# Performance work log

Measured on AMD Instinct MI355X. Metric: run time of the kernel, lower is better.

## Reference

```python
import jax, jax.numpy as jnp
import numpy as np
from jax import lax

N_NODES = 100000
N_EDGES = 600000  # even: edges stored as consecutive reverse pairs
NODE_F = 64
EDGE_F = 16
EDGE_H = 128
NODE_H = 128
NUM_STEPS = 6


def setup_inputs() -> dict:
    key = jax.random.key(0)
    ks = jax.random.split(key, 16)
    # paired reverse edges: edge 2k is (src,dst), edge 2k+1 is (dst,src)
    src = jax.random.randint(ks[0], (N_EDGES // 2,), 0, N_NODES, dtype=jnp.int32)
    dst = jax.random.randint(ks[1], (N_EDGES // 2,), 0, N_NODES, dtype=jnp.int32)
    from_nodes = jnp.stack([src, dst], axis=1).reshape(-1)
    to_nodes = jnp.stack([dst, src], axis=1).reshape(-1)
    edges = jnp.stack([from_nodes, to_nodes], axis=0)
    return {
        "node_features": jax.random.normal(ks[2], (N_NODES, NODE_F), jnp.float32),
        "edge_features": jax.random.normal(ks[3], (N_EDGES, EDGE_F), jnp.float32),
        "edge_hiddens": jnp.zeros((N_EDGES, EDGE_H), jnp.float32),
        "edges": edges,
        "W1_w": jax.random.normal(ks[4], (NODE_F, EDGE_H), jnp.float32) / np.sqrt(NODE_F),
        "W1_b": jnp.zeros((EDGE_H,), jnp.float32),
        "W2_w": jax.random.normal(ks[5], (EDGE_F, EDGE_H), jnp.float32) / np.sqrt(EDGE_F),
        "W2_b": jnp.zeros((EDGE_H,), jnp.float32),
        "W3_w": jax.random.normal(ks[6], (EDGE_H, EDGE_H), jnp.float32) / np.sqrt(EDGE_H),
        "W3_b": jnp.zeros((EDGE_H,), jnp.float32),
        "U1_w": jax.random.normal(ks[7], (NODE_F, NODE_H), jnp.float32) / np.sqrt(NODE_F),
        "U1_b": jnp.zeros((NODE_H,), jnp.float32),
        "U2_w": jax.random.normal(ks[8], (EDGE_H, NODE_H), jnp.float32) / np.sqrt(EDGE_H),
        "U2_b": jnp.zeros((NODE_H,), jnp.float32),
    }


def reference(node_features, edge_features, edge_hiddens, edges,
              W1_w, W1_b, W2_w, W2_b, W3_w, W3_b, U1_w, U1_b, U2_w, U2_b):
    from_nodes = edges[0]
    to_nodes = edges[1]
    n_edges = edges.shape[1]
    # backlink of edge i is its reverse pair: even i -> i+1, odd i -> i-1
    idx = jnp.arange(n_edges)
    backlink = idx + ((idx + 1) % 2) * 2 - 1

    # loop-invariant terms
    W1_x_u = (node_features @ W1_w + W1_b)[from_nodes]     # [E, EH]
    W2_x_uv = edge_features @ W2_w + W2_b                  # [E, EH]

    def step(h, _):
        # sum edge hiddens by source node, gather back per-edge, drop backlink
        s = jax.ops.segment_sum(h, from_nodes, num_segments=N_NODES)  # [N, EH]
        wu = s[from_nodes] - h[backlink]                               # [E, EH]
        h_new = jax.nn.relu(W1_x_u + W2_x_uv + (wu @ W3_w + W3_b))
        return h_new, None

    edge_h, _ = lax.scan(step, edge_hiddens, None, length=NUM_STEPS)

    U1_x_u = node_features @ U1_w + U1_b                   # [N, NH]
    U2_vu = edge_h @ U2_w + U2_b                           # [E, NH]
    agg = jax.ops.segment_sum(U2_vu, to_nodes, num_segments=N_NODES)
    node_hiddens = jax.nn.relu(U1_x_u + agg)               # [N, NH]
    return node_hiddens
```

## Files before the change

kernel.cpp:

```cpp
#include <hip/hip_runtime.h>
#include <hip/hip_bf16.h>

#define N_NODES 100000
#define N_EDGES 600000
#define SCAN_BLOCKS ((N_NODES + 255) / 256)

typedef __bf16 bf16;
typedef __bf16 bf16x2 __attribute__((ext_vector_type(2)));
typedef __bf16 bf16x4 __attribute__((ext_vector_type(4)));
typedef __bf16 bf16x8 __attribute__((ext_vector_type(8)));
typedef float f32x4 __attribute__((ext_vector_type(4)));

__global__ void deg_hist(const int* __restrict__ from, int* __restrict__ deg, int E) {
    int e = blockIdx.x * blockDim.x + threadIdx.x;
    if (e < E) atomicAdd(&deg[from[e]], 1);
}

__global__ __launch_bounds__(256) void block_sums(
    const int* __restrict__ deg, int* __restrict__ bsum)
{
    __shared__ int s[256];
    int i = blockIdx.x * 256 + threadIdx.x;
    s[threadIdx.x] = (i < N_NODES) ? deg[i] : 0;
    __syncthreads();
    for (int st = 128; st > 0; st >>= 1) {
        if (threadIdx.x < st) s[threadIdx.x] += s[threadIdx.x + st];
        __syncthreads();
    }
    if (threadIdx.x == 0) bsum[blockIdx.x] = s[0];
}

__global__ __launch_bounds__(256) void scan_partials(
    const int* __restrict__ bsum, int* __restrict__ bpref, int* __restrict__ off)
{
    __shared__ int s[SCAN_BLOCKS];
    for (int i = threadIdx.x; i < SCAN_BLOCKS; i += 256) s[i] = bsum[i];
    __syncthreads();
    if (threadIdx.x == 0) {
        int run = 0;
        for (int i = 0; i < SCAN_BLOCKS; i++) { int t = s[i]; s[i] = run; run += t; }
        off[N_NODES] = run;
    }
    __syncthreads();
    for (int i = threadIdx.x; i < SCAN_BLOCKS; i += 256) bpref[i] = s[i];
}

__global__ __launch_bounds__(256) void block_scan(
    const int* __restrict__ deg, const int* __restrict__ bpref,
    int* __restrict__ off, int* __restrict__ cursor)
{
    __shared__ int s[256];
    int i = blockIdx.x * 256 + threadIdx.x;
    int v = (i < N_NODES) ? deg[i] : 0;
    s[threadIdx.x] = v;
    __syncthreads();
    for (int st = 1; st < 256; st <<= 1) {
        int x = (threadIdx.x >= st) ? s[threadIdx.x - st] : 0;
        __syncthreads();
        s[threadIdx.x] += x;
        __syncthreads();
    }
    if (i < N_NODES) {
        int o = bpref[blockIdx.x] + s[threadIdx.x] - v;
        off[i] = o;
        cursor[i] = o;
    }
}

__global__ void scatter_csr(const int* __restrict__ from, int* __restrict__ cursor,
                            int* __restrict__ se, int E) {
    int e = blockIdx.x * blockDim.x + threadIdx.x;
    if (e < E) {
        int p = atomicAdd(&cursor[from[e]], 1);
        se[p] = e;
    }
}

__global__ __launch_bounds__(256) void node_gemm(
    const float* __restrict__ A, const float* __restrict__ B,
    const float* __restrict__ bias, float* __restrict__ C, int M)
{
    __shared__ float As[16][65];
    __shared__ float Bs[16][128];
    int row0 = blockIdx.x * 64;
    int tid = threadIdx.x;
    int tx = tid & 15, ty = tid >> 4;
    float acc[4][8];
    #pragma unroll
    for (int i = 0; i < 4; i++)
        #pragma unroll
        for (int j = 0; j < 8; j++) acc[i][j] = 0.f;

    for (int kk = 0; kk < 64; kk += 16) {
        int m  = tid >> 2;
        int k4 = (tid & 3) * 4;
        float4 v = make_float4(0.f, 0.f, 0.f, 0.f);
        if (row0 + m < M)
            v = *(const float4*)(A + (size_t)(row0 + m) * 64 + kk + k4);
        As[k4 + 0][m] = v.x; As[k4 + 1][m] = v.y;
        As[k4 + 2][m] = v.z; As[k4 + 3][m] = v.w;
        #pragma unroll
        for (int t = 0; t < 2; t++) {
            int id = tid + t * 256;
            int k = id >> 5, n4 = (id & 31) * 4;
            *(float4*)(&Bs[k][n4]) = *(const float4*)(B + (size_t)(kk + k) * 128 + n4);
        }
        __syncthreads();
        #pragma unroll
        for (int k = 0; k < 16; k++) {
            float a[4], b[8];
            #pragma unroll
            for (int i = 0; i < 4; i++) a[i] = As[k][ty * 4 + i];
            #pragma unroll
            for (int j = 0; j < 8; j++) b[j] = Bs[k][tx + j * 16];
            #pragma unroll
            for (int i = 0; i < 4; i++)
                #pragma unroll
                for (int j = 0; j < 8; j++) acc[i][j] += a[i] * b[j];
        }
        __syncthreads();
    }
    #pragma unroll
    for (int i = 0; i < 4; i++) {
        int r = row0 + ty * 4 + i;
        if (r < M) {
            #pragma unroll
            for (int j = 0; j < 8; j++) {
                int c = tx + j * 16;
                C[(size_t)r * 128 + c] = acc[i][j] + bias[c];
            }
        }
    }
}

__global__ __launch_bounds__(256) void base_v2(
    const float* __restrict__ nodeW1, const int* __restrict__ from,
    const float* __restrict__ ef, const float* __restrict__ W2,
    const float* __restrict__ W2b, const float* __restrict__ W3b,
    bf16* __restrict__ baseB)
{
    int tid = threadIdx.x;
    int c0 = (tid & 31) * 4;
    int sub = tid >> 5;
    float4 w[16];
    #pragma unroll
    for (int k = 0; k < 16; k++) w[k] = *(const float4*)(W2 + k * 128 + c0);
    float4 bias;
    {
        float4 a = *(const float4*)(W2b + c0);
        float4 b = *(const float4*)(W3b + c0);
        bias = make_float4(a.x + b.x, a.y + b.y, a.z + b.z, a.w + b.w);
    }
    #pragma unroll 1
    for (int it = 0; it < 64; ++it) {
        int e = blockIdx.x * 512 + it * 8 + sub;
        if (e >= N_EDGES) break;
        const float* efr = ef + (size_t)e * 16;
        float4 nv = *(const float4*)(nodeW1 + (size_t)from[e] * 128 + c0);
        float4 acc = make_float4(bias.x + nv.x, bias.y + nv.y,
                                 bias.z + nv.z, bias.w + nv.w);
        #pragma unroll
        for (int k = 0; k < 16; k++) {
            float s = efr[k];
            acc.x += s * w[k].x; acc.y += s * w[k].y;
            acc.z += s * w[k].z; acc.w += s * w[k].w;
        }
        bf16x4 o;
        o[0] = (bf16)acc.x; o[1] = (bf16)acc.y; o[2] = (bf16)acc.z; o[3] = (bf16)acc.w;
        *(bf16x4*)(baseB + (size_t)e * 128 + c0) = o;
    }
}

__global__ __launch_bounds__(256) void prep_weights(
    const float* __restrict__ W3, const float* __restrict__ U2,
    bf16* __restrict__ W3T, bf16* __restrict__ U2T)
{
    int i = blockIdx.x * 256 + threadIdx.x;
    if (i < 128 * 128) {
        int k = i >> 7, n = i & 127;
        W3T[n * 128 + k] = (bf16)W3[k * 128 + n];
        U2T[n * 128 + k] = (bf16)U2[k * 128 + n];
    }
}

__global__ __launch_bounds__(256) void edge_mfma(
    const bf16* __restrict__ baseB, const bf16* __restrict__ gbuf,
    const bf16* __restrict__ Sprev, const int* __restrict__ from,
    const bf16* __restrict__ BT, bf16* __restrict__ gout, int fused)
{
    __shared__ bf16 As[64][136];
    __shared__ bf16 Bs[128][136];
    int row0 = blockIdx.x * 64;
    int tid = threadIdx.x;

    #pragma unroll
    for (int t = 0; t < 8; t++) {
        int cid = tid + t * 256;
        int brow = cid >> 4, bcol = (cid & 15) * 8;
        *(bf16x8*)&Bs[brow][bcol] = *(const bf16x8*)(BT + (size_t)brow * 128 + bcol);
    }

    int r  = tid >> 2;
    int e  = row0 + r;
    int c0 = (tid & 3) * 32;
    if (!fused) {
        #pragma unroll
        for (int cc = 0; cc < 32; cc += 8) {
            int c = c0 + cc;
            bf16x8 bb = *(const bf16x8*)(baseB + (size_t)e * 128 + c);
            bf16x8 o;
            #pragma unroll
            for (int j = 0; j < 8; j++) o[j] = (bf16)fmaxf((float)bb[j], 0.f);
            *(bf16x8*)&As[r][c] = o;
        }
    } else {
        int fe = from[e];
        const bf16* sr = Sprev + (size_t)fe * 128;
        const bf16* gr = gbuf + (size_t)(e ^ 1) * 128;
        #pragma unroll
        for (int cc = 0; cc < 32; cc += 8) {
            int c = c0 + cc;
            bf16x8 bb = *(const bf16x8*)(baseB + (size_t)e * 128 + c);
            bf16x8 gg = *(const bf16x8*)(gr + c);
            bf16x8 ss = *(const bf16x8*)(sr + c);
            bf16x8 o;
            #pragma unroll
            for (int j = 0; j < 8; j++) {
                float v = (float)bb[j] + (float)ss[j] - (float)gg[j];
                o[j] = (bf16)fmaxf(v, 0.f);
            }
            *(bf16x8*)&As[r][c] = o;
        }
    }
    __syncthreads();

    int wave = tid >> 6, lane = tid & 63;
    int quad = lane >> 4, mr = lane & 15;
    int m0 = wave * 16;
    f32x4 acc[8];
    #pragma unroll
    for (int n = 0; n < 8; n++) acc[n] = (f32x4){0.f, 0.f, 0.f, 0.f};
    #pragma unroll
    for (int kt = 0; kt < 4; kt++) {
        bf16x8 a = *(const bf16x8*)&As[m0 + mr][kt * 32 + quad * 8];
        #pragma unroll
        for (int n = 0; n < 8; n++) {
            bf16x8 b = *(const bf16x8*)&Bs[n * 16 + mr][kt * 32 + quad * 8];
            acc[n] = __builtin_amdgcn_mfma_f32_16x16x32_bf16(a, b, acc[n], 0, 0, 0);
        }
    }

    #pragma unroll
    for (int n = 0; n < 8; n++) {
        int col = n * 16 + mr;
        #pragma unroll
        for (int reg = 0; reg < 4; reg++) {
            int rr = row0 + m0 + quad * 4 + reg;
            gout[(size_t)rr * 128 + col] = (bf16)acc[n][reg];
        }
    }
}

template<int FINAL>
__global__ __launch_bounds__(256) void segsum(
    const bf16* __restrict__ g, const int* __restrict__ off,
    const int* __restrict__ se, bf16* __restrict__ Sout, float* __restrict__ aggout)
{
    int n = blockIdx.x * 4 + (threadIdx.x >> 6);
    if (n >= N_NODES) return;
    int lane = threadIdx.x & 63;
    int o0 = off[n], o1 = off[n + 1];
    float a0 = 0.f, a1 = 0.f;
    for (int i = o0; i < o1; ++i) {
        int e = se[i] ^ FINAL;
        bf16x2 v = *(const bf16x2*)(g + (size_t)e * 128 + lane * 2);
        a0 += (float)v[0];
        a1 += (float)v[1];
    }
    if (FINAL) {
        *(float2*)(aggout + (size_t)n * 128 + lane * 2) = make_float2(a0, a1);
    } else {
        bf16x2 o; o[0] = (bf16)a0; o[1] = (bf16)a1;
        *(bf16x2*)(Sout + (size_t)n * 128 + lane * 2) = o;
    }
}

__global__ __launch_bounds__(256) void final_out(
    const float* __restrict__ U1x, const float* __restrict__ agg,
    const int* __restrict__ deg, const float* __restrict__ U2b,
    float* __restrict__ out)
{
    int gid = blockIdx.x * 256 + threadIdx.x;
    int n  = gid >> 5;
    if (n >= N_NODES) return;
    int c4 = gid & 31;
    float d = (float)deg[n];
    float4 a  = *(const float4*)(U1x + (size_t)n * 128 + c4 * 4);
    float4 ag = *(const float4*)(agg + (size_t)n * 128 + c4 * 4);
    float4 ub = *(const float4*)(U2b + c4 * 4);
    float4 r;
    r.x = fmaxf(a.x + ag.x + d * ub.x, 0.f);
    r.y = fmaxf(a.y + ag.y + d * ub.y, 0.f);
    r.z = fmaxf(a.z + ag.z + d * ub.z, 0.f);
    r.w = fmaxf(a.w + ag.w + d * ub.w, 0.f);
    *(float4*)(out + (size_t)n * 128 + c4 * 4) = r;
}

extern "C" void kernel_launch(void* const* d_in, const int* in_sizes, int n_in,
                              void* d_out, int out_size, void* d_ws, size_t ws_size,
                              hipStream_t stream) {
    const float* nf  = (const float*)d_in[0];
    const float* ef  = (const float*)d_in[1];
    const int* edges = (const int*)d_in[3];
    const int* from  = edges;
    const float* W1w = (const float*)d_in[4];
    const float* W1b = (const float*)d_in[5];
    const float* W2w = (const float*)d_in[6];
    const float* W2b = (const float*)d_in[7];
    const float* W3w = (const float*)d_in[8];
    const float* W3b = (const float*)d_in[9];
    const float* U1w = (const float*)d_in[10];
    const float* U1b = (const float*)d_in[11];
    const float* U2w = (const float*)d_in[12];
    const float* U2b = (const float*)d_in[13];
    float* out = (float*)d_out;

    const size_t NODE_MAT = (size_t)N_NODES * 128;
    const size_t EDGE_MAT = (size_t)N_EDGES * 128;
    char* w = (char*)d_ws;
    float* nodeW1 = (float*)w; w += NODE_MAT * 4;
    float* agg    = (float*)w; w += NODE_MAT * 4;
    bf16*  S      = (bf16*)w;  w += NODE_MAT * 2;
    bf16*  baseB  = (bf16*)w;  w += EDGE_MAT * 2;
    bf16*  gbuf   = (bf16*)w;  w += EDGE_MAT * 2;
    bf16*  W3T    = (bf16*)w;  w += 128 * 128 * 2;
    bf16*  U2T    = (bf16*)w;  w += 128 * 128 * 2;
    int*   deg    = (int*)w;   w += (size_t)N_NODES * 4;
    int*   off    = (int*)w;   w += (size_t)(N_NODES + 1) * 4;
    int*   cursor = (int*)w;   w += (size_t)N_NODES * 4;
    int*   bsum   = (int*)w;   w += (size_t)SCAN_BLOCKS * 4;
    int*   bpref  = (int*)w;   w += (size_t)SCAN_BLOCKS * 4;
    int*   se     = (int*)w;   w += (size_t)N_EDGES * 4;

    hipMemsetAsync(deg, 0, (size_t)N_NODES * 4, stream);
    deg_hist<<<(N_EDGES + 255) / 256, 256, 0, stream>>>(from, deg, N_EDGES);
    block_sums<<<SCAN_BLOCKS, 256, 0, stream>>>(deg, bsum);
    scan_partials<<<1, 256, 0, stream>>>(bsum, bpref, off);
    block_scan<<<SCAN_BLOCKS, 256, 0, stream>>>(deg, bpref, off, cursor);
    scatter_csr<<<(N_EDGES + 255) / 256, 256, 0, stream>>>(from, cursor, se, N_EDGES);

    prep_weights<<<(128 * 128 + 255) / 256, 256, 0, stream>>>(W3w, U2w, W3T, U2T);
    node_gemm<<<(N_NODES + 63) / 64, 256, 0, stream>>>(nf, W1w, W1b, nodeW1, N_NODES);
    base_v2<<<(N_EDGES + 511) / 512, 256, 0, stream>>>(nodeW1, from, ef, W2w, W2b, W3b, baseB);

    edge_mfma<<<N_EDGES / 64, 256, 0, stream>>>(baseB, gbuf, S, from, W3T, gbuf, 0);
    segsum<0><<<(N_NODES + 3) / 4, 256, 0, stream>>>(gbuf, off, se, S, agg);
    for (int it = 1; it < 5; ++it) {
        edge_mfma<<<N_EDGES / 64, 256, 0, stream>>>(baseB, gbuf, S, from, W3T, gbuf, 1);
        segsum<0><<<(N_NODES + 3) / 4, 256, 0, stream>>>(gbuf, off, se, S, agg);
    }
    edge_mfma<<<N_EDGES / 64, 256, 0, stream>>>(baseB, gbuf, S, from, U2T, gbuf, 1);
    segsum<1><<<(N_NODES + 3) / 4, 256, 0, stream>>>(gbuf, off, se, S, agg);

    node_gemm<<<(N_NODES + 63) / 64, 256, 0, stream>>>(nf, U1w, U1b, nodeW1, N_NODES);
    final_out<<<(N_NODES * 32 + 255) / 256, 256, 0, stream>>>(nodeW1, agg, deg, U2b, out);
}
```

Before: 1.777 ms.

## Permute edges into CSR order so segment sums stream contiguous rows

Edges are reordered by source node via a rank map, so base terms and per-step hidden buffers live in CSR-sorted order. The per-step segment sum then reads contiguous rows instead of gathering through the edge list. The reverse-edge read becomes an indexed gather through a precomputed backlink map. Hidden buffers are double-buffered, which also removes in-place read/write hazards. This adds index-map kernels and an extra edge-sized buffer.

```diff
diff --git a/kernel.cpp b/kernel.cpp
--- a/kernel.cpp
+++ b/kernel.cpp
@@ -68,11 +68,23 @@
 }
 
 __global__ void scatter_csr(const int* __restrict__ from, int* __restrict__ cursor,
-                            int* __restrict__ se, int E) {
+                            int* __restrict__ se, int* __restrict__ rank, int E) {
     int e = blockIdx.x * blockDim.x + threadIdx.x;
     if (e < E) {
         int p = atomicAdd(&cursor[from[e]], 1);
         se[p] = e;
+        rank[e] = p;
+    }
+}
+
+__global__ void make_maps(const int* __restrict__ se, const int* __restrict__ from,
+                          const int* __restrict__ rank,
+                          int* __restrict__ fromP, int* __restrict__ backP, int E) {
+    int i = blockIdx.x * blockDim.x + threadIdx.x;
+    if (i < E) {
+        int e = se[i];
+        fromP[i] = from[e];
+        backP[i] = rank[e ^ 1];
     }
 }
 
@@ -133,11 +145,11 @@
     }
 }
 
-__global__ __launch_bounds__(256) void base_v2(
-    const float* __restrict__ nodeW1, const int* __restrict__ from,
-    const float* __restrict__ ef, const float* __restrict__ W2,
-    const float* __restrict__ W2b, const float* __restrict__ W3b,
-    bf16* __restrict__ baseB)
+__global__ __launch_bounds__(256) void base_sorted(
+    const float* __restrict__ nodeW1, const int* __restrict__ fromP,
+    const int* __restrict__ se, const float* __restrict__ ef,
+    const float* __restrict__ W2, const float* __restrict__ W2b,
+    const float* __restrict__ W3b, bf16* __restrict__ baseP)
 {
     int tid = threadIdx.x;
     int c0 = (tid & 31) * 4;
@@ -153,10 +165,10 @@
     }
     #pragma unroll 1
     for (int it = 0; it < 64; ++it) {
-        int e = blockIdx.x * 512 + it * 8 + sub;
-        if (e >= N_EDGES) break;
-        const float* efr = ef + (size_t)e * 16;
-        float4 nv = *(const float4*)(nodeW1 + (size_t)from[e] * 128 + c0);
+        int i = blockIdx.x * 512 + it * 8 + sub;
+        if (i >= N_EDGES) break;
+        const float* efr = ef + (size_t)se[i] * 16;
+        float4 nv = *(const float4*)(nodeW1 + (size_t)fromP[i] * 128 + c0);
         float4 acc = make_float4(bias.x + nv.x, bias.y + nv.y,
                                  bias.z + nv.z, bias.w + nv.w);
         #pragma unroll
@@ -167,7 +179,7 @@
         }
         bf16x4 o;
         o[0] = (bf16)acc.x; o[1] = (bf16)acc.y; o[2] = (bf16)acc.z; o[3] = (bf16)acc.w;
-        *(bf16x4*)(baseB + (size_t)e * 128 + c0) = o;
+        *(bf16x4*)(baseP + (size_t)i * 128 + c0) = o;
     }
 }
 
@@ -183,10 +195,11 @@
     }
 }
 
-__global__ __launch_bounds__(256) void edge_mfma(
-    const bf16* __restrict__ baseB, const bf16* __restrict__ gbuf,
-    const bf16* __restrict__ Sprev, const int* __restrict__ from,
-    const bf16* __restrict__ BT, bf16* __restrict__ gout, int fused)
+__global__ __launch_bounds__(256) void edge_mfma_s(
+    const bf16* __restrict__ baseP, const bf16* __restrict__ gin,
+    const bf16* __restrict__ S, const int* __restrict__ fromP,
+    const int* __restrict__ backP, const bf16* __restrict__ BT,
+    bf16* __restrict__ gout, int fused)
 {
     __shared__ bf16 As[64][136];
     __shared__ bf16 Bs[128][136];
@@ -201,26 +214,25 @@
     }
 
     int r  = tid >> 2;
-    int e  = row0 + r;
+    int i  = row0 + r;
     int c0 = (tid & 3) * 32;
     if (!fused) {
         #pragma unroll
         for (int cc = 0; cc < 32; cc += 8) {
             int c = c0 + cc;
-            bf16x8 bb = *(const bf16x8*)(baseB + (size_t)e * 128 + c);
+            bf16x8 bb = *(const bf16x8*)(baseP + (size_t)i * 128 + c);
             bf16x8 o;
             #pragma unroll
             for (int j = 0; j < 8; j++) o[j] = (bf16)fmaxf((float)bb[j], 0.f);
             *(bf16x8*)&As[r][c] = o;
         }
     } else {
-        int fe = from[e];
-        const bf16* sr = Sprev + (size_t)fe * 128;
-        const bf16* gr = gbuf + (size_t)(e ^ 1) * 128;
+        const bf16* sr = S + (size_t)fromP[i] * 128;
+        const bf16* gr = gin + (size_t)backP[i] * 128;
         #pragma unroll
         for (int cc = 0; cc < 32; cc += 8) {
             int c = c0 + cc;
-            bf16x8 bb = *(const bf16x8*)(baseB + (size_t)e * 128 + c);
+            bf16x8 bb = *(const bf16x8*)(baseP + (size_t)i * 128 + c);
             bf16x8 gg = *(const bf16x8*)(gr + c);
             bf16x8 ss = *(const bf16x8*)(sr + c);
             bf16x8 o;
@@ -261,10 +273,8 @@
     }
 }
 
-template<int FINAL>
-__global__ __launch_bounds__(256) void segsum(
-    const bf16* __restrict__ g, const int* __restrict__ off,
-    const int* __restrict__ se, bf16* __restrict__ Sout, float* __restrict__ aggout)
+__global__ __launch_bounds__(256) void segsum_stream(
+    const bf16* __restrict__ g, const int* __restrict__ off, bf16* __restrict__ S)
 {
     int n = blockIdx.x * 4 + (threadIdx.x >> 6);
     if (n >= N_NODES) return;
@@ -272,17 +282,30 @@
     int o0 = off[n], o1 = off[n + 1];
     float a0 = 0.f, a1 = 0.f;
     for (int i = o0; i < o1; ++i) {
-        int e = se[i] ^ FINAL;
+        bf16x2 v = *(const bf16x2*)(g + (size_t)i * 128 + lane * 2);
+        a0 += (float)v[0];
+        a1 += (float)v[1];
+    }
+    bf16x2 o; o[0] = (bf16)a0; o[1] = (bf16)a1;
+    *(bf16x2*)(S + (size_t)n * 128 + lane * 2) = o;
+}
+
+__global__ __launch_bounds__(256) void segsum_final(
+    const bf16* __restrict__ g, const int* __restrict__ off,
+    const int* __restrict__ backP, float* __restrict__ agg)
+{
+    int n = blockIdx.x * 4 + (threadIdx.x >> 6);
+    if (n >= N_NODES) return;
+    int lane = threadIdx.x & 63;
+    int o0 = off[n], o1 = off[n + 1];
+    float a0 = 0.f, a1 = 0.f;
+    for (int i = o0; i < o1; ++i) {
+        int e = backP[i];
         bf16x2 v = *(const bf16x2*)(g + (size_t)e * 128 + lane * 2);
         a0 += (float)v[0];
         a1 += (float)v[1];
     }
-    if (FINAL) {
-        *(float2*)(aggout + (size_t)n * 128 + lane * 2) = make_float2(a0, a1);
-    } else {
-        bf16x2 o; o[0] = (bf16)a0; o[1] = (bf16)a1;
-        *(bf16x2*)(Sout + (size_t)n * 128 + lane * 2) = o;
-    }
+    *(float2*)(agg + (size_t)n * 128 + lane * 2) = make_float2(a0, a1);
 }
 
 __global__ __launch_bounds__(256) void final_out(
@@ -331,8 +354,9 @@
     float* nodeW1 = (float*)w; w += NODE_MAT * 4;
     float* agg    = (float*)w; w += NODE_MAT * 4;
     bf16*  S      = (bf16*)w;  w += NODE_MAT * 2;
-    bf16*  baseB  = (bf16*)w;  w += EDGE_MAT * 2;
-    bf16*  gbuf   = (bf16*)w;  w += EDGE_MAT * 2;
+    bf16*  baseP  = (bf16*)w;  w += EDGE_MAT * 2;
+    bf16*  g0     = (bf16*)w;  w += EDGE_MAT * 2;
+    bf16*  g1     = (bf16*)w;  w += EDGE_MAT * 2;
     bf16*  W3T    = (bf16*)w;  w += 128 * 128 * 2;
     bf16*  U2T    = (bf16*)w;  w += 128 * 128 * 2;
     int*   deg    = (int*)w;   w += (size_t)N_NODES * 4;
@@ -341,26 +365,38 @@
     int*   bsum   = (int*)w;   w += (size_t)SCAN_BLOCKS * 4;
     int*   bpref  = (int*)w;   w += (size_t)SCAN_BLOCKS * 4;
     int*   se     = (int*)w;   w += (size_t)N_EDGES * 4;
+    int*   rank   = (int*)w;   w += (size_t)N_EDGES * 4;
+    int*   fromP  = (int*)w;   w += (size_t)N_EDGES * 4;
+    int*   backP  = (int*)w;   w += (size_t)N_EDGES * 4;
 
     hipMemsetAsync(deg, 0, (size_t)N_NODES * 4, stream);
     deg_hist<<<(N_EDGES + 255) / 256, 256, 0, stream>>>(from, deg, N_EDGES);
     block_sums<<<SCAN_BLOCKS, 256, 0, stream>>>(deg, bsum);
     scan_partials<<<1, 256, 0, stream>>>(bsum, bpref, off);
     block_scan<<<SCAN_BLOCKS, 256, 0, stream>>>(deg, bpref, off, cursor);
-    scatter_csr<<<(N_EDGES + 255) / 256, 256, 0, stream>>>(from, cursor, se, N_EDGES);
+    scatter_csr<<<(N_EDGES + 255) / 256, 256, 0, stream>>>(from, cursor, se, rank, N_EDGES);
+    make_maps<<<(N_EDGES + 255) / 256, 256, 0, stream>>>(se, from, rank, fromP, backP, N_EDGES);
 
     prep_weights<<<(128 * 128 + 255) / 256, 256, 0, stream>>>(W3w, U2w, W3T, U2T);
     node_gemm<<<(N_NODES + 63) / 64, 256, 0, stream>>>(nf, W1w, W1b, nodeW1, N_NODES);
-    base_v2<<<(N_EDGES + 511) / 512, 256, 0, stream>>>(nodeW1, from, ef, W2w, W2b, W3b, baseB);
-
-    edge_mfma<<<N_EDGES / 64, 256, 0, stream>>>(baseB, gbuf, S, from, W3T, gbuf, 0);
-    segsum<0><<<(N_NODES + 3) / 4, 256, 0, stream>>>(gbuf, off, se, S, agg);
+    base_sorted<<<(N_EDGES + 511) / 512, 256, 0, stream>>>(
+        nodeW1, fromP, se, ef, W2w, W2b, W3b, baseP);
+
+    bf16* G[2] = {g0, g1};
+    edge_mfma_s<<<N_EDGES / 64, 256, 0, stream>>>(
+        baseP, G[0], S, fromP, backP, W3T, G[0], 0);
+    segsum_stream<<<(N_NODES + 3) / 4, 256, 0, stream>>>(G[0], off, S);
+    int cur = 0;
     for (int it = 1; it < 5; ++it) {
-        edge_mfma<<<N_EDGES / 64, 256, 0, stream>>>(baseB, gbuf, S, from, W3T, gbuf, 1);
-        segsum<0><<<(N_NODES + 3) / 4, 256, 0, stream>>>(gbuf, off, se, S, agg);
-    }
-    edge_mfma<<<N_EDGES / 64, 256, 0, stream>>>(baseB, gbuf, S, from, U2T, gbuf, 1);
-    segsum<1><<<(N_NODES + 3) / 4, 256, 0, stream>>>(gbuf, off, se, S, agg);
+        edge_mfma_s<<<N_EDGES / 64, 256, 0, stream>>>(
+            baseP, G[cur], S, fromP, backP, W3T, G[cur ^ 1], 1);
+        cur ^= 1;
+        segsum_stream<<<(N_NODES + 3) / 4, 256, 0, stream>>>(G[cur], off, S);
+    }
+    edge_mfma_s<<<N_EDGES / 64, 256, 0, stream>>>(
+        baseP, G[cur], S, fromP, backP, U2T, G[cur ^ 1], 1);
+    cur ^= 1;
+    segsum_final<<<(N_NODES + 3) / 4, 256, 0, stream>>>(G[cur], off, backP, agg);
 
     node_gemm<<<(N_NODES + 63) / 64, 256, 0, stream>>>(nf, U1w, U1b, nodeW1, N_NODES);
     final_out<<<(N_NODES * 32 + 255) / 256, 256, 0, stream>>>(nodeW1, agg, deg, U2b, out);
```

After: 1.690 ms. 4.9% less time.
